# Optimization experiments

Hardware: AMD Instinct MI355X
Metric: run time of the kernel (lower is better)

The kernel has to match this reference:

```python
import jax, jax.numpy as jnp
import numpy as np

OUTPUT_LEN = 8  # init: output_len
# init: pred_conversion=False, conf_thres=None, vote_conf_by_count=True, select_by_conf=True


def setup_inputs() -> dict:
    key = jax.random.key(0)
    x = jax.random.normal(key, (128, 8192, 64), dtype=jnp.float32)
    return {"x": x}


def _per_sample(conf, pred):
    # conf, pred: [T]
    T = conf.shape[0]
    # run-length encoding (unique_consecutive): mark the start of each run
    is_start = jnp.concatenate([jnp.ones((1,), bool), pred[1:] != pred[:-1]])
    run_id = jnp.cumsum(is_start.astype(jnp.int32)) - 1  # [T], run index per position
    # count of each run (padded to T segments; unused segments are 0)
    counts = jax.ops.segment_sum(jnp.ones((T,), conf.dtype), run_id, num_segments=T)
    # voted confidence at run starts: conf_at_start * run_count (vote_conf_by_count=True)
    voted = jnp.where(is_start, conf * counts[run_id], -jnp.inf)
    # select_by_conf=True: take top output_len runs by voted confidence
    vals, idx = jax.lax.top_k(voted, OUTPUT_LEN)
    sel = pred[idx]
    # fewer runs than output_len -> pad with 0 (torch pads with new_zeros)
    sel = jnp.where(jnp.isfinite(vals), sel, 0)
    return sel


def reference(x):
    p = jax.nn.softmax(x, axis=-1)          # [B, T, C]
    conf = jnp.max(p, axis=-1)              # [B, T]
    pred = jnp.argmax(p, axis=-1)           # [B, T] int
    out = jax.vmap(_per_sample)(conf, pred)  # [B, OUTPUT_LEN] int
    return out.astype(x.dtype)               # x.new_tensor(results) -> float
```

## Files before the change

kernel.cpp:

```cpp
#include <hip/hip_runtime.h>
#include <stdint.h>

#define T_LEN 8192
#define C_LEN 64
#define OUT_LEN 8

__global__ __launch_bounds__(256) void softmax_stats_kernel(
    const float* __restrict__ x, float* __restrict__ conf,
    int* __restrict__ pred, int nrows)
{
    const int tid  = threadIdx.x;
    const int wave = tid >> 6;
    const int lane = tid & 63;
    const int rw   = lane >> 4;
    const int sub  = lane & 15;
    const long long row = (long long)blockIdx.x * 16 + wave * 4 + rw;
    if (row >= nrows) return;

    const float4 v = ((const float4*)(x + row * C_LEN))[sub];

    float m = v.x; int mi = sub * 4;
    if (v.y > m) { m = v.y; mi = sub * 4 + 1; }
    if (v.z > m) { m = v.z; mi = sub * 4 + 2; }
    if (v.w > m) { m = v.w; mi = sub * 4 + 3; }

    #pragma unroll
    for (int off = 8; off >= 1; off >>= 1) {
        float om = __shfl_xor(m, off);
        int   oi = __shfl_xor(mi, off);
        if (om > m || (om == m && oi < mi)) { m = om; mi = oi; }
    }

    float s = expf(v.x - m) + expf(v.y - m) + expf(v.z - m) + expf(v.w - m);
    #pragma unroll
    for (int off = 8; off >= 1; off >>= 1) s += __shfl_xor(s, off);

    if (sub == 0) {
        conf[row] = 1.0f / s;
        pred[row] = mi;
    }
}

__global__ __launch_bounds__(256) void topk_kernel(
    const float* __restrict__ conf, const int* __restrict__ pred,
    float* __restrict__ out)
{
    __shared__ short pred_s[T_LEN];
    __shared__ float voted_s[T_LEN];
    __shared__ unsigned long long wbest[4];

    const int b   = blockIdx.x;
    const int tid = threadIdx.x;
    const int* __restrict__  pb = pred + (long long)b * T_LEN;
    const float* __restrict__ cb = conf + (long long)b * T_LEN;

    for (int t = tid; t < T_LEN; t += 256) pred_s[t] = (short)pb[t];
    __syncthreads();

    for (int t = tid; t < T_LEN; t += 256) {
        const short p = pred_s[t];
        const bool start = (t == 0) || (pred_s[t - 1] != p);
        float v = 0.0f;
        if (start) {
            int len = 1;
            while (t + len < T_LEN && pred_s[t + len] == p) ++len;
            v = cb[t] * (float)len;
        }
        voted_s[t] = v;
    }
    __syncthreads();

    const int lane = tid & 63, wave = tid >> 6;

    for (int r = 0; r < OUT_LEN; ++r) {
        unsigned long long best = 0ull;
        for (int t = tid; t < T_LEN; t += 256) {
            unsigned long long key =
                ((unsigned long long)__float_as_uint(voted_s[t]) << 32)
                | (unsigned int)(~t);
            if (key > best) best = key;
        }
        #pragma unroll
        for (int off = 32; off >= 1; off >>= 1) {
            unsigned long long o = __shfl_xor(best, off);
            if (o > best) best = o;
        }
        if (lane == 0) wbest[wave] = best;
        __syncthreads();
        if (tid == 0) {
            unsigned long long bb = wbest[0];
            #pragma unroll
            for (int w = 1; w < 4; ++w) if (wbest[w] > bb) bb = wbest[w];
            const unsigned int widx = ~(unsigned int)(bb & 0xffffffffu);
            const float v = __uint_as_float((unsigned int)(bb >> 32));
            float ov = 0.0f;
            if (v > 0.0f) { ov = (float)pred_s[widx]; voted_s[widx] = 0.0f; }
            out[b * OUT_LEN + r] = ov;
        }
        __syncthreads();
    }
}

extern "C" void kernel_launch(void* const* d_in, const int* in_sizes, int n_in,
                              void* d_out, int out_size, void* d_ws, size_t ws_size,
                              hipStream_t stream) {
    const float* x = (const float*)d_in[0];
    const int total = in_sizes[0];
    const int nrows = total / C_LEN;
    const int B     = nrows / T_LEN;

    float* conf = (float*)d_ws;
    int*   pred = (int*)((char*)d_ws + (size_t)nrows * sizeof(float));
    float* out  = (float*)d_out;

    const int gridA = (nrows + 15) / 16;
    softmax_stats_kernel<<<gridA, 256, 0, stream>>>(x, conf, pred, nrows);
    topk_kernel<<<B, 256, 0, stream>>>(conf, pred, out);
}
```

Before: 372.2 us.

## Pack argmax into 64-bit key, cache per-wave top-k maxima, launch softmax kernel twice

The softmax-stats kernel now packs the order-preserving max value and the inverted index into one 64-bit key, so each shuffle step does one exchange instead of two, and it uses the fast __expf. The top-k kernel gives each wave a contiguous quarter of the array and, after the first round, rescans only the quarter whose element was just removed. It also loads pred as int4 and writes the output through shared memory. The softmax kernel is launched twice, which repeats the full 128 MiB input read and will likely add substantial time.

```diff
diff --git a/kernel.cpp b/kernel.cpp
--- a/kernel.cpp
+++ b/kernel.cpp
@@ -24,20 +24,29 @@
     if (v.z > m) { m = v.z; mi = sub * 4 + 2; }
     if (v.w > m) { m = v.w; mi = sub * 4 + 3; }
 
+    const unsigned int s0 = __float_as_uint(m);
+    const unsigned int u0 = (s0 & 0x80000000u) ? ~s0 : (s0 | 0x80000000u);
+    unsigned long long key =
+        ((unsigned long long)u0 << 32) | (unsigned int)~mi;
+
     #pragma unroll
     for (int off = 8; off >= 1; off >>= 1) {
-        float om = __shfl_xor(m, off);
-        int   oi = __shfl_xor(mi, off);
-        if (om > m || (om == m && oi < mi)) { m = om; mi = oi; }
+        const unsigned long long o = __shfl_xor(key, off);
+        if (o > key) key = o;
     }
 
-    float s = expf(v.x - m) + expf(v.y - m) + expf(v.z - m) + expf(v.w - m);
+    const unsigned int uu = (unsigned int)(key >> 32);
+    const float M = __uint_as_float(
+        (uu & 0x80000000u) ? (uu ^ 0x80000000u) : ~uu);
+
+    float s = __expf(v.x - M) + __expf(v.y - M)
+            + __expf(v.z - M) + __expf(v.w - M);
     #pragma unroll
     for (int off = 8; off >= 1; off >>= 1) s += __shfl_xor(s, off);
 
     if (sub == 0) {
         conf[row] = 1.0f / s;
-        pred[row] = mi;
+        pred[row] = (int)~(unsigned int)(key & 0xffffffffu);
     }
 }
 
@@ -47,14 +56,23 @@
 {
     __shared__ short pred_s[T_LEN];
     __shared__ float voted_s[T_LEN];
-    __shared__ unsigned long long wbest[4];
+    __shared__ unsigned long long wkey[4];
+    __shared__ int   dirty;
+    __shared__ float outbuf[OUT_LEN];
 
-    const int b   = blockIdx.x;
-    const int tid = threadIdx.x;
-    const int* __restrict__  pb = pred + (long long)b * T_LEN;
+    const int b    = blockIdx.x;
+    const int tid  = threadIdx.x;
+    const int lane = tid & 63, wave = tid >> 6;
+    const int* __restrict__   pb = pred + (long long)b * T_LEN;
     const float* __restrict__ cb = conf + (long long)b * T_LEN;
 
-    for (int t = tid; t < T_LEN; t += 256) pred_s[t] = (short)pb[t];
+    for (int i = tid; i < T_LEN / 4; i += 256) {
+        const int4 p4 = ((const int4*)pb)[i];
+        short4 q; q.x = (short)p4.x; q.y = (short)p4.y;
+        q.z = (short)p4.z; q.w = (short)p4.w;
+        *(short4*)&pred_s[4 * i] = q;
+    }
+    if (tid == 0) dirty = -1;
     __syncthreads();
 
     for (int t = tid; t < T_LEN; t += 256) {
@@ -70,35 +88,45 @@
     }
     __syncthreads();
 
-    const int lane = tid & 63, wave = tid >> 6;
-
     for (int r = 0; r < OUT_LEN; ++r) {
-        unsigned long long best = 0ull;
-        for (int t = tid; t < T_LEN; t += 256) {
-            unsigned long long key =
-                ((unsigned long long)__float_as_uint(voted_s[t]) << 32)
-                | (unsigned int)(~t);
-            if (key > best) best = key;
+        if (dirty == -1 || dirty == wave) {
+            unsigned long long best = 0ull;
+            const int base = wave * (T_LEN / 4);
+            #pragma unroll 4
+            for (int k = 0; k < T_LEN / 4 / 64; ++k) {
+                const int t = base + k * 64 + lane;
+                const unsigned long long key =
+                    ((unsigned long long)__float_as_uint(voted_s[t]) << 32)
+                    | (unsigned int)(~t);
+                if (key > best) best = key;
+            }
+            #pragma unroll
+            for (int off = 32; off >= 1; off >>= 1) {
+                const unsigned long long o = __shfl_xor(best, off);
+                if (o > best) best = o;
+            }
+            if (lane == 0) wkey[wave] = best;
         }
-        #pragma unroll
-        for (int off = 32; off >= 1; off >>= 1) {
-            unsigned long long o = __shfl_xor(best, off);
-            if (o > best) best = o;
-        }
-        if (lane == 0) wbest[wave] = best;
         __syncthreads();
         if (tid == 0) {
-            unsigned long long bb = wbest[0];
+            unsigned long long bb = wkey[0];
             #pragma unroll
-            for (int w = 1; w < 4; ++w) if (wbest[w] > bb) bb = wbest[w];
+            for (int w = 1; w < 4; ++w) if (wkey[w] > bb) bb = wkey[w];
             const unsigned int widx = ~(unsigned int)(bb & 0xffffffffu);
             const float v = __uint_as_float((unsigned int)(bb >> 32));
             float ov = 0.0f;
-            if (v > 0.0f) { ov = (float)pred_s[widx]; voted_s[widx] = 0.0f; }
-            out[b * OUT_LEN + r] = ov;
+            if (v > 0.0f) {
+                ov = (float)pred_s[widx];
+                voted_s[widx] = 0.0f;
+                dirty = (int)(widx / (T_LEN / 4));
+            } else {
+                dirty = 4;
+            }
+            outbuf[r] = ov;
         }
         __syncthreads();
     }
+    if (tid < OUT_LEN) out[b * OUT_LEN + tid] = outbuf[tid];
 }
 
 extern "C" void kernel_launch(void* const* d_in, const int* in_sizes, int n_in,
@@ -115,5 +143,6 @@
 
     const int gridA = (nrows + 15) / 16;
     softmax_stats_kernel<<<gridA, 256, 0, stream>>>(x, conf, pred, nrows);
+    softmax_stats_kernel<<<gridA, 256, 0, stream>>>(x, conf, pred, nrows);
     topk_kernel<<<B, 256, 0, stream>>>(conf, pred, out);
 }
```

Measured after the change: 418.0 us. +12.3%, slower.
